# Kernel optimization log

Measured on AMD Instinct MI355X. Metric: run time of the kernel, lower is better.

The kernel has to match this reference:

```python
import jax, jax.numpy as jnp
import numpy as np

NUM_EXPERTS = 8
TOP_K = 2
N_EMBD = 1024
D_FFN = 2048  # 4*N_EMBD // TOP_K, already multiple of BLOCK_N=128
BLOCK_M = 128
NORM_TOPK = True


def setup_inputs() -> dict:
    key = jax.random.key(0)
    k1, k2, k3 = jax.random.split(key, 3)
    x = jax.random.normal(k1, (2, 2048, N_EMBD), dtype=jnp.float32)
    router_w = jax.random.normal(k2, (NUM_EXPERTS, N_EMBD), dtype=jnp.float32) * 0.02
    w1 = jax.random.normal(k3, (N_EMBD, D_FFN * NUM_EXPERTS), dtype=jnp.float32) * 0.02
    return {"x": x, "router_w": router_w, "w1": w1}


def reference(x, router_w, w1):
    B, S, H = x.shape
    x_flat = x.reshape(-1, H)                                   # [T, H]
    router_logits = x_flat @ router_w.T                         # [T, E]
    probs = jax.nn.softmax(router_logits.astype(jnp.float32), axis=-1)
    rweights, sel = jax.lax.top_k(probs, TOP_K)                 # [T, k]
    if NORM_TOPK:
        rweights = rweights / rweights.sum(axis=-1, keepdims=True)
    rweights = rweights.astype(x.dtype)

    # repeat_interleave tokens top_k times, then stable-sort by expert id
    x_rep = jnp.repeat(x_flat, TOP_K, axis=0)                   # [M, H]
    sel_rep = sel.reshape(-1)                                   # [M]
    rw_rep = rweights.reshape(-1, 1)                            # [M, 1]
    order = jnp.argsort(sel_rep, stable=True)                   # expert-sort permutation
    x_grouped = x_rep[order]                                    # [M, H]
    sel_sorted = sel_rep[order]                                 # [M]
    rw_sorted = rw_rep[order]                                   # [M, 1]

    M = x_grouped.shape[0]
    nblk = M // BLOCK_M                                         # M divisible by BLOCK_M by construction
    # SDD kernel: expert of the first row of each BLOCK_M block selects w1 slice
    block_expert = sel_sorted[::BLOCK_M]                        # [nblk] == col_indices_ptr
    w1e = w1.reshape(H, NUM_EXPERTS, D_FFN)                     # w1[:, e*D:(e+1)*D] == w1e[:, e, :]
    w_blk = jnp.take(w1e, block_expert, axis=1)                 # [H, nblk, D]
    x_blk = x_grouped.reshape(nblk, BLOCK_M, H)                 # [nblk, Bm, H]
    block_sparse = jnp.einsum('bmh,hbd->bmd', x_blk, w_blk).reshape(M, D_FFN)

    block_sparse = jax.nn.gelu(block_sparse, approximate=False) * rw_sorted
    return block_sparse, router_logits
```

## Files before the change

kernel.cpp:

```cpp
#include <hip/hip_runtime.h>
#include <hip/hip_bf16.h>
#include <cmath>

typedef float f32x16 __attribute__((ext_vector_type(16)));
typedef __bf16 bf16x8 __attribute__((ext_vector_type(8)));
typedef __bf16 bf16x4 __attribute__((ext_vector_type(4)));

#define NE 8
#define H 1024
#define DF 2048
#define WCOLS 16384
#define NTOK 4096
#define MROWS 8192
#define NBLK 64
#define TILE_E 4096

typedef const __attribute__((address_space(1))) unsigned int glb_u32;
typedef __attribute__((address_space(3))) unsigned int lds_u32;

__device__ __forceinline__ void async_load16(const void* g, void* l) {
    __builtin_amdgcn_global_load_lds((glb_u32*)g, (lds_u32*)l, 16, 0, 0);
}

__global__ __launch_bounds__(256) void prep_kernel(
    const float* __restrict__ x, const float* __restrict__ rw,
    const float* __restrict__ w1,
    float* __restrict__ logits, int* __restrict__ sel, float* __restrict__ rwn,
    __bf16* __restrict__ xb, __bf16* __restrict__ Wt)
{
    __shared__ float tile[32][132];
    int b = blockIdx.x;
    int tid = threadIdx.x;
    if (b < 1024) {
        int tok  = b * 4 + (tid >> 6);
        int lane = tid & 63;
        const float* xr = x + (size_t)tok * H;
        __bf16* xbr = xb + (size_t)tok * H;
        float acc[NE];
#pragma unroll
        for (int e = 0; e < NE; ++e) acc[e] = 0.f;
#pragma unroll
        for (int it = 0; it < 4; ++it) {
            int k = (it * 64 + lane) * 4;
            float4 xv = *(const float4*)(xr + k);
            bf16x4 xc;
            xc[0] = (__bf16)xv.x; xc[1] = (__bf16)xv.y;
            xc[2] = (__bf16)xv.z; xc[3] = (__bf16)xv.w;
            *(bf16x4*)(xbr + k) = xc;
#pragma unroll
            for (int e = 0; e < NE; ++e) {
                float4 wv = *(const float4*)(rw + e * H + k);
                acc[e] += xv.x * wv.x + xv.y * wv.y + xv.z * wv.z + xv.w * wv.w;
            }
        }
#pragma unroll
        for (int e = 0; e < NE; ++e) {
            float v = acc[e];
#pragma unroll
            for (int off = 32; off > 0; off >>= 1) v += __shfl_xor(v, off, 64);
            acc[e] = v;
        }
        if (lane == 0) {
#pragma unroll
            for (int e = 0; e < NE; ++e) logits[tok * NE + e] = acc[e];
            int i1 = 0; float m1 = acc[0];
#pragma unroll
            for (int e = 1; e < NE; ++e) if (acc[e] > m1) { m1 = acc[e]; i1 = e; }
            int i2 = -1; float m2 = -INFINITY;
#pragma unroll
            for (int e = 0; e < NE; ++e) if (e != i1 && acc[e] > m2) { m2 = acc[e]; i2 = e; }
            float e2 = expf(m2 - m1);
            float inv = 1.f / (1.f + e2);
            sel[tok * 2]     = i1;  sel[tok * 2 + 1] = i2;
            rwn[tok * 2]     = inv; rwn[tok * 2 + 1] = e2 * inv;
        }
        return;
    }
    int g  = b - 1024;
    int c  = g >> 5;
    int kb = g & 31;
    int kk = tid >> 3;
    int cc = (tid & 7) * 16;
    const float* src = w1 + (size_t)(kb * 32 + kk) * WCOLS + c * 128 + cc;
#pragma unroll
    for (int i = 0; i < 4; ++i) {
        float4 v = *(const float4*)(src + i * 4);
        *(float4*)&tile[kk][cc + i * 4] = v;
    }
    __syncthreads();
    int n = tid >> 1, kc0 = (tid & 1) * 16;
    bf16x8 o0, o1;
#pragma unroll
    for (int i = 0; i < 8; ++i) {
        o0[i] = (__bf16)tile[kc0 + i][n];
        o1[i] = (__bf16)tile[kc0 + 8 + i][n];
    }
    __bf16* dst = Wt + (size_t)g * TILE_E + n * 32 + kc0;
    *(bf16x8*)dst       = o0;
    *(bf16x8*)(dst + 8) = o1;
}

__global__ __launch_bounds__(1024) void sort_kernel(
    const int* __restrict__ sel, const float* __restrict__ rwn,
    int* __restrict__ stok, float* __restrict__ srw, int* __restrict__ bexp)
{
    __shared__ int cnt[NE][1024];
    __shared__ int wtot[NE][2];
    __shared__ int ebase[NE + 1];
    int t = threadIdx.x;
    int selv[8];
    int lc[NE];
#pragma unroll
    for (int e = 0; e < NE; ++e) lc[e] = 0;
    int base = t * 8;
#pragma unroll
    for (int j = 0; j < 8; ++j) { selv[j] = sel[base + j]; lc[selv[j]]++; }
#pragma unroll
    for (int e = 0; e < NE; ++e) cnt[e][t] = lc[e];
    __syncthreads();
    int g = t >> 7, j = t & 127, jl = j & 63;
    int s = 0, pre[8];
#pragma unroll
    for (int i = 0; i < 8; ++i) { pre[i] = s; s += cnt[g][j * 8 + i]; }
    int inc = s;
#pragma unroll
    for (int d = 1; d < 64; d <<= 1) {
        int v = __shfl_up(inc, d, 64);
        if (jl >= d) inc += v;
    }
    if (jl == 63) wtot[g][j >> 6] = inc;
    __syncthreads();
    int add = (j >= 64) ? wtot[g][0] : 0;
    int excl = inc - s + add;
#pragma unroll
    for (int i = 0; i < 8; ++i) cnt[g][j * 8 + i] = excl + pre[i];
    __syncthreads();
    if (t == 0) {
        int acc = 0;
        for (int e = 0; e < NE; ++e) { ebase[e] = acc; acc += wtot[e][0] + wtot[e][1]; }
        ebase[NE] = acc;
    }
    __syncthreads();
    int off[NE];
#pragma unroll
    for (int e = 0; e < NE; ++e) off[e] = ebase[e] + cnt[e][t];
#pragma unroll
    for (int j2 = 0; j2 < 8; ++j2) {
        int i = base + j2;
        int e = selv[j2];
        int pos = off[e]++;
        stok[pos] = i >> 1;
        srw[pos]  = rwn[i];
    }
    __syncthreads();
    if (t < NBLK) {
        int r = t * 128;
        int e = 0;
        while (e < NE - 1 && r >= ebase[e + 1]) ++e;
        bexp[t] = e;
    }
}

__global__ __launch_bounds__(256, 4) void moe_gemm(
    const __bf16* __restrict__ xb, const __bf16* __restrict__ Wt,
    const int* __restrict__ stok, const float* __restrict__ srw,
    const int* __restrict__ bexp, float* __restrict__ out)
{
    __shared__ __align__(16) __bf16 As[2][4096];
    __shared__ __align__(16) __bf16 Bs[2][4096];
    __shared__ int   tokS[128];
    __shared__ float rwS[128];

    int g = blockIdx.x;
    int by = (g & 7) * 8 + ((g >> 3) & 7);
    int bx = g >> 6;
    int tid = threadIdx.x;
    if (tid < 128) {
        tokS[tid] = stok[by * 128 + tid];
        rwS[tid]  = srw[by * 128 + tid];
    }
    int e = bexp[by];
    __syncthreads();

    int lane = tid & 63;
    int wv   = tid >> 6;
    int rsub = lane >> 2;
    int kcE  = (lane & 3) * 8;
    int r0   = wv * 32 + rsub;
    int r1   = r0 + 16;

    const __bf16* aS0 = xb + (size_t)tokS[r0] * H + kcE;
    const __bf16* aS1 = xb + (size_t)tokS[r1] * H + kcE;
    const __bf16* bT  = Wt + (size_t)(e * 16 + bx) * 32 * TILE_E + wv * 1024 + lane * 8;
    __bf16* aL[2] = { &As[0][wv * 1024], &As[1][wv * 1024] };
    __bf16* bL[2] = { &Bs[0][wv * 1024], &Bs[1][wv * 1024] };

    int wm  = (wv & 1) * 64;
    int wn  = (wv >> 1) * 64;
    int l32 = lane & 31;
    int khi = (lane >> 5) * 8;

    f32x16 acc[2][2];
#pragma unroll
    for (int i = 0; i < 2; ++i)
#pragma unroll
        for (int j = 0; j < 2; ++j)
#pragma unroll
            for (int r = 0; r < 16; ++r) acc[i][j][r] = 0.f;

    async_load16(aS0, aL[0]);
    async_load16(aS1, aL[0] + 512);
    async_load16(bT,  bL[0]);
    async_load16(bT + 512, bL[0] + 512);

    for (int kb = 0; kb < 32; ++kb) {
        int cur = kb & 1;
        __syncthreads();
        if (kb < 31) {
            const __bf16* aN0 = aS0 + (kb + 1) * 32;
            const __bf16* aN1 = aS1 + (kb + 1) * 32;
            const __bf16* bN  = bT + (size_t)(kb + 1) * TILE_E;
            async_load16(aN0, aL[1 - cur]);
            async_load16(aN1, aL[1 - cur] + 512);
            async_load16(bN,  bL[1 - cur]);
            async_load16(bN + 512, bL[1 - cur] + 512);
        }
        bf16x8 af[2][2], bfr[2][2];
#pragma unroll
        for (int h = 0; h < 2; ++h) {
#pragma unroll
            for (int ti = 0; ti < 2; ++ti)
                af[ti][h] = *(const bf16x8*)&As[cur][(wm + ti * 32 + l32) * 32 + h * 16 + khi];
#pragma unroll
            for (int tj = 0; tj < 2; ++tj)
                bfr[tj][h] = *(const bf16x8*)&Bs[cur][(wn + tj * 32 + l32) * 32 + h * 16 + khi];
        }
#pragma unroll
        for (int h = 0; h < 2; ++h)
#pragma unroll
            for (int ti = 0; ti < 2; ++ti)
#pragma unroll
                for (int tj = 0; tj < 2; ++tj)
                    acc[ti][tj] = __builtin_amdgcn_mfma_f32_32x32x16_bf16(
                        af[ti][h], bfr[tj][h], acc[ti][tj], 0, 0, 0);
    }

    int rowh = (lane >> 5) * 4;
#pragma unroll
    for (int ti = 0; ti < 2; ++ti)
#pragma unroll
        for (int tj = 0; tj < 2; ++tj)
#pragma unroll
            for (int reg = 0; reg < 16; ++reg) {
                int row = (reg & 3) + 8 * (reg >> 2) + rowh;
                int m = wm + ti * 32 + row;
                int n = wn + tj * 32 + l32;
                float val = acc[ti][tj][reg];
                float u = 0.7978845608028654f * val * (1.f + 0.044715f * val * val);
                float t = __expf(-2.f * fabsf(u));
                float th = (1.f - t) / (1.f + t);
                th = u < 0.f ? -th : th;
                float gv = 0.5f * val * (1.f + th) * rwS[m];
                out[(size_t)(by * 128 + m) * DF + bx * 128 + n] = gv;
            }
}

extern "C" void kernel_launch(void* const* d_in, const int* in_sizes, int n_in,
                              void* d_out, int out_size, void* d_ws, size_t ws_size,
                              hipStream_t stream) {
    (void)in_sizes; (void)n_in; (void)out_size; (void)ws_size;
    const float* x        = (const float*)d_in[0];
    const float* router_w = (const float*)d_in[1];
    const float* w1       = (const float*)d_in[2];
    float* out    = (float*)d_out;
    float* logits = out + (size_t)MROWS * DF;

    char* ws    = (char*)d_ws;
    int*   sel  = (int*)(ws);
    float* rwn  = (float*)(ws + 0x8000);
    int*   stok = (int*)(ws + 0x10000);
    float* srw  = (float*)(ws + 0x18000);
    int*   bexp = (int*)(ws + 0x20000);
    __bf16* xb  = (__bf16*)(ws + (1 << 20));
    __bf16* Wt  = (__bf16*)(ws + (1 << 20) + (8 << 20));

    prep_kernel<<<5120, 256, 0, stream>>>(x, router_w, w1, logits, sel, rwn, xb, Wt);
    sort_kernel<<<1, 1024, 0, stream>>>(sel, rwn, stok, srw, bexp);
    moe_gemm<<<16 * NBLK, 256, 0, stream>>>(xb, Wt, stok, srw, bexp, out);
}
```

Measured before the change: 190.6 us.

## Widen GEMM tile to 128x256 and pre-swizzle weights into MFMA fragment layout

```diff
diff --git a/kernel.cpp b/kernel.cpp
--- a/kernel.cpp
+++ b/kernel.cpp
@@ -13,7 +13,7 @@
 #define NTOK 4096
 #define MROWS 8192
 #define NBLK 64
-#define TILE_E 4096
+
 
 typedef const __attribute__((address_space(1))) unsigned int glb_u32;
 typedef __attribute__((address_space(3))) unsigned int lds_u32;
@@ -95,9 +95,12 @@
         o0[i] = (__bf16)tile[kc0 + i][n];
         o1[i] = (__bf16)tile[kc0 + 8 + i][n];
     }
-    __bf16* dst = Wt + (size_t)g * TILE_E + n * 32 + kc0;
-    *(bf16x8*)dst       = o0;
-    *(bf16x8*)(dst + 8) = o1;
+    size_t tile_id = (size_t)(c >> 1) * 32 + kb;
+    int group  = (c & 1) * 4 + (n >> 5);
+    int chunk0 = kc0 >> 3;
+    __bf16* dst = Wt + tile_id * 8192 + group * 1024 + chunk0 * 256 + (n & 31) * 8;
+    *(bf16x8*)dst         = o0;
+    *(bf16x8*)(dst + 256) = o1;
 }
 
 __global__ __launch_bounds__(1024) void sort_kernel(
@@ -161,19 +164,19 @@
     }
 }
 
-__global__ __launch_bounds__(256, 4) void moe_gemm(
+__global__ __launch_bounds__(256, 2) void moe_gemm(
     const __bf16* __restrict__ xb, const __bf16* __restrict__ Wt,
     const int* __restrict__ stok, const float* __restrict__ srw,
     const int* __restrict__ bexp, float* __restrict__ out)
 {
     __shared__ __align__(16) __bf16 As[2][4096];
-    __shared__ __align__(16) __bf16 Bs[2][4096];
+    __shared__ __align__(16) __bf16 Bs[2][8192];
     __shared__ int   tokS[128];
     __shared__ float rwS[128];
 
     int g = blockIdx.x;
-    int by = (g & 7) * 8 + ((g >> 3) & 7);
-    int bx = g >> 6;
+    int by  = (g & 7) * 8 + ((g >> 3) & 7);
+    int bxp = g >> 6;
     int tid = threadIdx.x;
     if (tid < 128) {
         tokS[tid] = stok[by * 128 + tid];
@@ -184,85 +187,87 @@
 
     int lane = tid & 63;
     int wv   = tid >> 6;
-    int rsub = lane >> 2;
-    int kcE  = (lane & 3) * 8;
-    int r0   = wv * 32 + rsub;
-    int r1   = r0 + 16;
-
-    const __bf16* aS0 = xb + (size_t)tokS[r0] * H + kcE;
-    const __bf16* aS1 = xb + (size_t)tokS[r1] * H + kcE;
-    const __bf16* bT  = Wt + (size_t)(e * 16 + bx) * 32 * TILE_E + wv * 1024 + lane * 8;
-    __bf16* aL[2] = { &As[0][wv * 1024], &As[1][wv * 1024] };
-    __bf16* bL[2] = { &Bs[0][wv * 1024], &Bs[1][wv * 1024] };
-
-    int wm  = (wv & 1) * 64;
-    int wn  = (wv >> 1) * 64;
-    int l32 = lane & 31;
-    int khi = (lane >> 5) * 8;
-
-    f32x16 acc[2][2];
+    int l32  = lane & 31;
+    int hi   = lane >> 5;
+
+    const __bf16* aSrc = xb + (size_t)tokS[wv * 32 + l32] * H + hi * 8;
+    __bf16* aDst0 = &As[0][wv * 1024 + lane * 8];
+    __bf16* aDst1 = &As[1][wv * 1024 + lane * 8];
+
+    const __bf16* bSrc = Wt + (size_t)(e * 8 + bxp) * 32 * 8192 + wv * 2048 + lane * 8;
+    __bf16* bDst0 = &Bs[0][wv * 2048 + lane * 8];
+    __bf16* bDst1 = &Bs[1][wv * 2048 + lane * 8];
+
+    int wm = (wv & 1) * 64;
+    int wn = (wv >> 1) * 128;
+    int ag = (wv & 1) * 2;
+    int bg = (wv >> 1) * 4;
+
+    f32x16 acc[2][4];
 #pragma unroll
     for (int i = 0; i < 2; ++i)
 #pragma unroll
-        for (int j = 0; j < 2; ++j)
+        for (int j = 0; j < 4; ++j)
 #pragma unroll
             for (int r = 0; r < 16; ++r) acc[i][j][r] = 0.f;
 
-    async_load16(aS0, aL[0]);
-    async_load16(aS1, aL[0] + 512);
-    async_load16(bT,  bL[0]);
-    async_load16(bT + 512, bL[0] + 512);
+#pragma unroll
+    for (int j = 0; j < 2; ++j) async_load16(aSrc + j * 16, aDst0 + j * 512);
+#pragma unroll
+    for (int j = 0; j < 4; ++j) async_load16(bSrc + j * 512, bDst0 + j * 512);
 
     for (int kb = 0; kb < 32; ++kb) {
         int cur = kb & 1;
         __syncthreads();
         if (kb < 31) {
-            const __bf16* aN0 = aS0 + (kb + 1) * 32;
-            const __bf16* aN1 = aS1 + (kb + 1) * 32;
-            const __bf16* bN  = bT + (size_t)(kb + 1) * TILE_E;
-            async_load16(aN0, aL[1 - cur]);
-            async_load16(aN1, aL[1 - cur] + 512);
-            async_load16(bN,  bL[1 - cur]);
-            async_load16(bN + 512, bL[1 - cur] + 512);
-        }
-        bf16x8 af[2][2], bfr[2][2];
+            const __bf16* aN = aSrc + (kb + 1) * 32;
+            const __bf16* bN = bSrc + (size_t)(kb + 1) * 8192;
+            __bf16* aD = cur ? aDst0 : aDst1;
+            __bf16* bD = cur ? bDst0 : bDst1;
+#pragma unroll
+            for (int j = 0; j < 2; ++j) async_load16(aN + j * 16, aD + j * 512);
+#pragma unroll
+            for (int j = 0; j < 4; ++j) async_load16(bN + j * 512, bD + j * 512);
+        }
+        bf16x8 af[2][2], bfr[4][2];
 #pragma unroll
         for (int h = 0; h < 2; ++h) {
 #pragma unroll
             for (int ti = 0; ti < 2; ++ti)
-                af[ti][h] = *(const bf16x8*)&As[cur][(wm + ti * 32 + l32) * 32 + h * 16 + khi];
-#pragma unroll
-            for (int tj = 0; tj < 2; ++tj)
-                bfr[tj][h] = *(const bf16x8*)&Bs[cur][(wn + tj * 32 + l32) * 32 + h * 16 + khi];
+                af[ti][h] = *(const bf16x8*)&As[cur][(ag + ti) * 1024 + (h * 2 + hi) * 256 + l32 * 8];
+#pragma unroll
+            for (int tj = 0; tj < 4; ++tj)
+                bfr[tj][h] = *(const bf16x8*)&Bs[cur][(bg + tj) * 1024 + (h * 2 + hi) * 256 + l32 * 8];
         }
 #pragma unroll
         for (int h = 0; h < 2; ++h)
 #pragma unroll
             for (int ti = 0; ti < 2; ++ti)
 #pragma unroll
-                for (int tj = 0; tj < 2; ++tj)
+                for (int tj = 0; tj < 4; ++tj)
                     acc[ti][tj] = __builtin_amdgcn_mfma_f32_32x32x16_bf16(
                         af[ti][h], bfr[tj][h], acc[ti][tj], 0, 0, 0);
     }
 
-    int rowh = (lane >> 5) * 4;
+    int rowh = hi * 4;
 #pragma unroll
     for (int ti = 0; ti < 2; ++ti)
 #pragma unroll
-        for (int tj = 0; tj < 2; ++tj)
-#pragma unroll
-            for (int reg = 0; reg < 16; ++reg) {
-                int row = (reg & 3) + 8 * (reg >> 2) + rowh;
-                int m = wm + ti * 32 + row;
-                int n = wn + tj * 32 + l32;
+        for (int reg = 0; reg < 16; ++reg) {
+            int row = (reg & 3) + 8 * (reg >> 2) + rowh;
+            int m = wm + ti * 32 + row;
+            float rw = rwS[m];
+            size_t ob = (size_t)(by * 128 + m) * DF + bxp * 256 + wn + l32;
+#pragma unroll
+            for (int tj = 0; tj < 4; ++tj) {
                 float val = acc[ti][tj][reg];
                 float u = 0.7978845608028654f * val * (1.f + 0.044715f * val * val);
                 float t = __expf(-2.f * fabsf(u));
                 float th = (1.f - t) / (1.f + t);
                 th = u < 0.f ? -th : th;
-                float gv = 0.5f * val * (1.f + th) * rwS[m];
-                out[(size_t)(by * 128 + m) * DF + bx * 128 + n] = gv;
+                out[ob + tj * 32] = 0.5f * val * (1.f + th) * rw;
             }
+        }
 }
 
 extern "C" void kernel_launch(void* const* d_in, const int* in_sizes, int n_in,
@@ -286,5 +291,5 @@
 
     prep_kernel<<<5120, 256, 0, stream>>>(x, router_w, w1, logits, sel, rwn, xb, Wt);
     sort_kernel<<<1, 1024, 0, stream>>>(sel, rwn, stok, srw, bexp);
-    moe_gemm<<<16 * NBLK, 256, 0, stream>>>(xb, Wt, stok, srw, bexp, out);
-}
+    moe_gemm<<<512, 256, 0, stream>>>(xb, Wt, stok, srw, bexp, out);
+}
```

Measured after the change: 188.1 us. No clear change (-1.3%).
